# Performance work log

Hardware: AMD Instinct MI355X
Metric: run time of the kernel (lower is better)

The kernel has to match this reference:

```python
import jax, jax.numpy as jnp
import numpy as np

N_HEADS = 16
HEAD_SIZE = 128


def setup_inputs() -> dict:
    key = jax.random.key(0)
    k1, k2, k3 = jax.random.split(key, 3)
    B, S, D = 2, 2048, N_HEADS * HEAD_SIZE
    return {
        "query": jax.random.normal(k1, (B, S, D), dtype=jnp.float32),
        "key": jax.random.normal(k2, (B, S, D), dtype=jnp.float32),
        "value": jax.random.normal(k3, (B, S, D), dtype=jnp.float32),
        "dropout_p": 0,
    }


def reference(query, key, value, dropout_p):
    B, S, D = query.shape
    H, Dh = N_HEADS, HEAD_SIZE
    scale = Dh ** (-0.5)
    q = query.reshape(B, S, H, Dh)
    k = key.reshape(B, S, H, Dh)
    v = value.reshape(B, S, H, Dh)
    # [B, H, Sq, Sk] attention scores
    scores = jnp.einsum("bqhd,bkhd->bhqk", q, k) * scale
    attn = jax.nn.softmax(scores, axis=-1)
    # dropout (deterministic baseline: p == 0 -> identity; inverted dropout otherwise)
    if dropout_p > 0:
        keep = 1.0 - dropout_p
        mask = jax.random.bernoulli(jax.random.key(42), keep, attn.shape)
        attn = jnp.where(mask, attn / keep, 0.0)
    out = jnp.einsum("bhqk,bkhd->bqhd", attn, v)
    return out.reshape(B, S, D)
```

## Files before the change

### kernel.cpp

```cpp
#include <hip/hip_runtime.h>
#include <hip/hip_bf16.h>

#define SEQ   2048
#define DD    2048
#define DH    128
#define NH    16
#define QBLK  128
#define KVBLK 64
#define NT    (SEQ / KVBLK)
#define NWAVE 8
#define BLK   (NWAVE * 64)

#define KSTR  136
#define VSTR  68
#define PSTR  72

typedef __attribute__((ext_vector_type(8))) short bf16x8;
typedef __attribute__((ext_vector_type(4))) short bf16x4;
typedef __attribute__((ext_vector_type(4))) float f32x4;
typedef __attribute__((ext_vector_type(4))) unsigned int u32x4;

__device__ __forceinline__ unsigned int cvt2(float lo, float hi) {
    __hip_bfloat162 h = __float22bfloat162_rn(make_float2(lo, hi));
    unsigned int u;
    __builtin_memcpy(&u, &h, 4);
    return u;
}

__device__ __forceinline__ u32x4 pack8(const float4 a, const float4 b) {
    u32x4 v;
    v[0] = cvt2(a.x, a.y);
    v[1] = cvt2(a.z, a.w);
    v[2] = cvt2(b.x, b.y);
    v[3] = cvt2(b.z, b.w);
    return v;
}

__device__ __forceinline__ unsigned short f2bf1(float f) {
    __hip_bfloat16 h = __float2bfloat16(f);
    unsigned short u;
    __builtin_memcpy(&u, &h, 2);
    return u;
}

__global__ __launch_bounds__(BLK, 4)
void fa_fwd(const float* __restrict__ qg, const float* __restrict__ kg,
            const float* __restrict__ vg, float* __restrict__ og) {
    __shared__ __align__(16) unsigned short Klds[KVBLK * KSTR];
    __shared__ __align__(16) unsigned short Vt[DH * VSTR];
    __shared__ __align__(16) unsigned short Plds[NWAVE * 16 * PSTR];

    const int tid  = threadIdx.x;
    const int w    = tid >> 6;
    const int lane = tid & 63;
    const int lo   = lane & 15;
    const int hi   = lane >> 4;

    const int bid = blockIdx.x;
    const int qt  = bid & 15;
    const int bh  = bid >> 4;
    const int b   = bh >> 4;
    const int h   = bh & 15;
    const int q0  = qt * QBLK;

    const size_t base = (size_t)b * SEQ * DD + (size_t)h * DH;

    bf16x8 qf[4];
    {
        const float* qp = qg + base + (size_t)(q0 + w * 16 + lo) * DD + hi * 8;
        #pragma unroll
        for (int kc = 0; kc < 4; ++kc) {
            float4 a = *(const float4*)(qp + kc * 32);
            float4 c = *(const float4*)(qp + kc * 32 + 4);
            qf[kc] = __builtin_bit_cast(bf16x8, pack8(a, c));
        }
    }

    f32x4 acco[8];
    const f32x4 zf = {0.f, 0.f, 0.f, 0.f};
    #pragma unroll
    for (int i = 0; i < 8; ++i) acco[i] = zf;
    float mrun[4] = {-1e30f, -1e30f, -1e30f, -1e30f};
    float lrun[4] = {0.f, 0.f, 0.f, 0.f};

    const float SCL = 0.08838834764831843f * 1.4426950408889634f;

    unsigned short* pw = Plds + w * 16 * PSTR;

    float4 kra[2], krc[2], vra[2], vrb[2];

    #define LOADT(T)                                                            \
        {                                                                       \
            const int k0_ = (T) * KVBLK;                                        \
            _Pragma("unroll")                                                   \
            for (int i = 0; i < 2; ++i) {                                       \
                int s = tid + i * BLK;                                          \
                const float* p = kg + base + (size_t)(k0_ + (s >> 4)) * DD + (s & 15) * 8; \
                kra[i] = *(const float4*)p;                                     \
                krc[i] = *(const float4*)(p + 4);                               \
                const float* pv = vg + base + (size_t)(k0_ + (s >> 5) * 2) * DD + (s & 31) * 4; \
                vra[i] = *(const float4*)pv;                                    \
                vrb[i] = *(const float4*)(pv + DD);                             \
            }                                                                   \
        }

    LOADT(0);

    for (int t = 0; t < NT; ++t) {
        __syncthreads();

        #pragma unroll
        for (int i = 0; i < 2; ++i) {
            int s = tid + i * BLK;
            *(u32x4*)&Klds[(s >> 4) * KSTR + (s & 15) * 8] = pack8(kra[i], krc[i]);
        }
        #pragma unroll
        for (int i = 0; i < 2; ++i) {
            int s  = tid + i * BLK;
            int kp = s >> 5;
            int c4 = s & 31;
            unsigned int w0 = cvt2(vra[i].x, vrb[i].x);
            unsigned int w1 = cvt2(vra[i].y, vrb[i].y);
            unsigned int w2 = cvt2(vra[i].z, vrb[i].z);
            unsigned int w3 = cvt2(vra[i].w, vrb[i].w);
            unsigned short* vt0 = &Vt[(c4 * 4) * VSTR + kp * 2];
            *(unsigned int*)(vt0)            = w0;
            *(unsigned int*)(vt0 + VSTR)     = w1;
            *(unsigned int*)(vt0 + 2 * VSTR) = w2;
            *(unsigned int*)(vt0 + 3 * VSTR) = w3;
        }

        if (t + 1 < NT) LOADT(t + 1);

        __syncthreads();

        f32x4 accs[4];
        #pragma unroll
        for (int nt = 0; nt < 4; ++nt) accs[nt] = zf;
        #pragma unroll
        for (int nt = 0; nt < 4; ++nt) {
            #pragma unroll
            for (int kk = 0; kk < 4; ++kk) {
                bf16x8 kb = *(const bf16x8*)&Klds[(nt * 16 + lo) * KSTR + kk * 32 + hi * 8];
                accs[nt] = __builtin_amdgcn_mfma_f32_16x16x32_bf16(qf[kk], kb, accs[nt], 0, 0, 0);
            }
        }

        float ps[4][4];
        float corr[4];
        #pragma unroll
        for (int r = 0; r < 4; ++r) {
            float s0 = accs[0][r] * SCL, s1 = accs[1][r] * SCL;
            float s2 = accs[2][r] * SCL, s3 = accs[3][r] * SCL;
            float tm = fmaxf(fmaxf(s0, s1), fmaxf(s2, s3));
            tm = fmaxf(tm, __shfl_xor(tm, 1));
            tm = fmaxf(tm, __shfl_xor(tm, 2));
            tm = fmaxf(tm, __shfl_xor(tm, 4));
            tm = fmaxf(tm, __shfl_xor(tm, 8));
            float mn = fmaxf(mrun[r], tm);
            float c  = exp2f(mrun[r] - mn);
            float p0 = exp2f(s0 - mn), p1 = exp2f(s1 - mn);
            float p2 = exp2f(s2 - mn), p3 = exp2f(s3 - mn);
            float ls = p0 + p1 + p2 + p3;
            ls += __shfl_xor(ls, 1);
            ls += __shfl_xor(ls, 2);
            ls += __shfl_xor(ls, 4);
            ls += __shfl_xor(ls, 8);
            lrun[r] = lrun[r] * c + ls;
            mrun[r] = mn;
            corr[r] = c;
            ps[0][r] = p0; ps[1][r] = p1; ps[2][r] = p2; ps[3][r] = p3;
        }
        #pragma unroll
        for (int d0 = 0; d0 < 8; ++d0) {
            acco[d0][0] *= corr[0]; acco[d0][1] *= corr[1];
            acco[d0][2] *= corr[2]; acco[d0][3] *= corr[3];
        }

        #pragma unroll
        for (int nt = 0; nt < 4; ++nt)
            #pragma unroll
            for (int r = 0; r < 4; ++r)
                pw[(hi * 4 + r) * PSTR + nt * 16 + lo] = f2bf1(ps[nt][r]);

        #pragma unroll
        for (int kc = 0; kc < 2; ++kc) {
            bf16x8 pa = *(const bf16x8*)&pw[lo * PSTR + kc * 32 + hi * 8];
            #pragma unroll
            for (int d0 = 0; d0 < 8; ++d0) {
                const unsigned short* vp = &Vt[(d0 * 16 + lo) * VSTR + kc * 32 + hi * 8];
                bf16x4 v0 = *(const bf16x4*)vp;
                bf16x4 v1 = *(const bf16x4*)(vp + 4);
                bf16x8 vb = __builtin_shufflevector(v0, v1, 0, 1, 2, 3, 4, 5, 6, 7);
                acco[d0] = __builtin_amdgcn_mfma_f32_16x16x32_bf16(pa, vb, acco[d0], 0, 0, 0);
            }
        }
    }

    float inv[4];
    #pragma unroll
    for (int r = 0; r < 4; ++r) inv[r] = 1.0f / lrun[r];
    float* op = og + base + (size_t)(q0 + w * 16 + hi * 4) * DD + lo;
    #pragma unroll
    for (int d0 = 0; d0 < 8; ++d0)
        #pragma unroll
        for (int r = 0; r < 4; ++r)
            op[(size_t)r * DD + d0 * 16] = acco[d0][r] * inv[r];
}

extern "C" void kernel_launch(void* const* d_in, const int* in_sizes, int n_in,
                              void* d_out, int out_size, void* d_ws, size_t ws_size,
                              hipStream_t stream) {
    const float* q = (const float*)d_in[0];
    const float* k = (const float*)d_in[1];
    const float* v = (const float*)d_in[2];
    float* o = (float*)d_out;
    const int B = in_sizes[0] / (SEQ * DD);
    dim3 grid(B * NH * (SEQ / QBLK));
    fa_fwd<<<grid, dim3(BLK), 0, stream>>>(q, k, v, o);
}
```

Before: 338.7 us.

## Process two 16-row query groups per wave with four waves per block

Each block drops from eight waves to four, and each wave now handles 32 query rows as two 16-row groups. Every K and V fragment read from LDS therefore feeds two MFMAs instead of one, halving LDS read traffic per unit of math. Each thread also stages twice as many K/V elements per tile. The cost is more registers per thread (two output accumulator sets, Q fragments and softmax state), so the launch bound drops to 2 blocks per CU, which may reduce occupancy and latency hiding.

```diff
diff --git a/kernel.cpp b/kernel.cpp
--- a/kernel.cpp
+++ b/kernel.cpp
@@ -8,7 +8,7 @@
 #define QBLK  128
 #define KVBLK 64
 #define NT    (SEQ / KVBLK)
-#define NWAVE 8
+#define NWAVE 4
 #define BLK   (NWAVE * 64)
 
 #define KSTR  136
@@ -43,12 +43,12 @@
     return u;
 }
 
-__global__ __launch_bounds__(BLK, 4)
+__global__ __launch_bounds__(BLK, 2)
 void fa_fwd(const float* __restrict__ qg, const float* __restrict__ kg,
             const float* __restrict__ vg, float* __restrict__ og) {
     __shared__ __align__(16) unsigned short Klds[KVBLK * KSTR];
     __shared__ __align__(16) unsigned short Vt[DH * VSTR];
-    __shared__ __align__(16) unsigned short Plds[NWAVE * 16 * PSTR];
+    __shared__ __align__(16) unsigned short Plds[NWAVE * 32 * PSTR];
 
     const int tid  = threadIdx.x;
     const int w    = tid >> 6;
@@ -65,35 +65,41 @@
 
     const size_t base = (size_t)b * SEQ * DD + (size_t)h * DH;
 
-    bf16x8 qf[4];
-    {
-        const float* qp = qg + base + (size_t)(q0 + w * 16 + lo) * DD + hi * 8;
+    bf16x8 qf[2][4];
+    #pragma unroll
+    for (int g = 0; g < 2; ++g) {
+        const float* qp = qg + base + (size_t)(q0 + w * 32 + g * 16 + lo) * DD + hi * 8;
         #pragma unroll
         for (int kc = 0; kc < 4; ++kc) {
             float4 a = *(const float4*)(qp + kc * 32);
             float4 c = *(const float4*)(qp + kc * 32 + 4);
-            qf[kc] = __builtin_bit_cast(bf16x8, pack8(a, c));
+            qf[g][kc] = __builtin_bit_cast(bf16x8, pack8(a, c));
         }
     }
 
-    f32x4 acco[8];
+    f32x4 acco[2][8];
     const f32x4 zf = {0.f, 0.f, 0.f, 0.f};
     #pragma unroll
-    for (int i = 0; i < 8; ++i) acco[i] = zf;
-    float mrun[4] = {-1e30f, -1e30f, -1e30f, -1e30f};
-    float lrun[4] = {0.f, 0.f, 0.f, 0.f};
+    for (int g = 0; g < 2; ++g)
+        #pragma unroll
+        for (int i = 0; i < 8; ++i) acco[g][i] = zf;
+    float mrun[2][4], lrun[2][4];
+    #pragma unroll
+    for (int g = 0; g < 2; ++g)
+        #pragma unroll
+        for (int r = 0; r < 4; ++r) { mrun[g][r] = -1e30f; lrun[g][r] = 0.f; }
 
     const float SCL = 0.08838834764831843f * 1.4426950408889634f;
 
-    unsigned short* pw = Plds + w * 16 * PSTR;
-
-    float4 kra[2], krc[2], vra[2], vrb[2];
+    unsigned short* pw = Plds + w * 32 * PSTR;
+
+    float4 kra[4], krc[4], vra[4], vrb[4];
 
     #define LOADT(T)                                                            \
         {                                                                       \
             const int k0_ = (T) * KVBLK;                                        \
             _Pragma("unroll")                                                   \
-            for (int i = 0; i < 2; ++i) {                                       \
+            for (int i = 0; i < 4; ++i) {                                       \
                 int s = tid + i * BLK;                                          \
                 const float* p = kg + base + (size_t)(k0_ + (s >> 4)) * DD + (s & 15) * 8; \
                 kra[i] = *(const float4*)p;                                     \
@@ -110,12 +116,12 @@
         __syncthreads();
 
         #pragma unroll
-        for (int i = 0; i < 2; ++i) {
+        for (int i = 0; i < 4; ++i) {
             int s = tid + i * BLK;
             *(u32x4*)&Klds[(s >> 4) * KSTR + (s & 15) * 8] = pack8(kra[i], krc[i]);
         }
         #pragma unroll
-        for (int i = 0; i < 2; ++i) {
+        for (int i = 0; i < 4; ++i) {
             int s  = tid + i * BLK;
             int kp = s >> 5;
             int c4 = s & 31;
@@ -134,78 +140,88 @@
 
         __syncthreads();
 
-        f32x4 accs[4];
-        #pragma unroll
-        for (int nt = 0; nt < 4; ++nt) accs[nt] = zf;
+        f32x4 accs[2][4];
+        #pragma unroll
+        for (int g = 0; g < 2; ++g)
+            #pragma unroll
+            for (int nt = 0; nt < 4; ++nt) accs[g][nt] = zf;
         #pragma unroll
         for (int nt = 0; nt < 4; ++nt) {
             #pragma unroll
             for (int kk = 0; kk < 4; ++kk) {
                 bf16x8 kb = *(const bf16x8*)&Klds[(nt * 16 + lo) * KSTR + kk * 32 + hi * 8];
-                accs[nt] = __builtin_amdgcn_mfma_f32_16x16x32_bf16(qf[kk], kb, accs[nt], 0, 0, 0);
-            }
-        }
-
-        float ps[4][4];
-        float corr[4];
-        #pragma unroll
-        for (int r = 0; r < 4; ++r) {
-            float s0 = accs[0][r] * SCL, s1 = accs[1][r] * SCL;
-            float s2 = accs[2][r] * SCL, s3 = accs[3][r] * SCL;
-            float tm = fmaxf(fmaxf(s0, s1), fmaxf(s2, s3));
-            tm = fmaxf(tm, __shfl_xor(tm, 1));
-            tm = fmaxf(tm, __shfl_xor(tm, 2));
-            tm = fmaxf(tm, __shfl_xor(tm, 4));
-            tm = fmaxf(tm, __shfl_xor(tm, 8));
-            float mn = fmaxf(mrun[r], tm);
-            float c  = exp2f(mrun[r] - mn);
-            float p0 = exp2f(s0 - mn), p1 = exp2f(s1 - mn);
-            float p2 = exp2f(s2 - mn), p3 = exp2f(s3 - mn);
-            float ls = p0 + p1 + p2 + p3;
-            ls += __shfl_xor(ls, 1);
-            ls += __shfl_xor(ls, 2);
-            ls += __shfl_xor(ls, 4);
-            ls += __shfl_xor(ls, 8);
-            lrun[r] = lrun[r] * c + ls;
-            mrun[r] = mn;
-            corr[r] = c;
-            ps[0][r] = p0; ps[1][r] = p1; ps[2][r] = p2; ps[3][r] = p3;
-        }
-        #pragma unroll
-        for (int d0 = 0; d0 < 8; ++d0) {
-            acco[d0][0] *= corr[0]; acco[d0][1] *= corr[1];
-            acco[d0][2] *= corr[2]; acco[d0][3] *= corr[3];
-        }
-
-        #pragma unroll
-        for (int nt = 0; nt < 4; ++nt)
-            #pragma unroll
-            for (int r = 0; r < 4; ++r)
-                pw[(hi * 4 + r) * PSTR + nt * 16 + lo] = f2bf1(ps[nt][r]);
+                accs[0][nt] = __builtin_amdgcn_mfma_f32_16x16x32_bf16(qf[0][kk], kb, accs[0][nt], 0, 0, 0);
+                accs[1][nt] = __builtin_amdgcn_mfma_f32_16x16x32_bf16(qf[1][kk], kb, accs[1][nt], 0, 0, 0);
+            }
+        }
+
+        #pragma unroll
+        for (int g = 0; g < 2; ++g) {
+            float ps[4][4];
+            float corr[4];
+            #pragma unroll
+            for (int r = 0; r < 4; ++r) {
+                float s0 = accs[g][0][r] * SCL, s1 = accs[g][1][r] * SCL;
+                float s2 = accs[g][2][r] * SCL, s3 = accs[g][3][r] * SCL;
+                float tm = fmaxf(fmaxf(s0, s1), fmaxf(s2, s3));
+                tm = fmaxf(tm, __shfl_xor(tm, 1));
+                tm = fmaxf(tm, __shfl_xor(tm, 2));
+                tm = fmaxf(tm, __shfl_xor(tm, 4));
+                tm = fmaxf(tm, __shfl_xor(tm, 8));
+                float mn = fmaxf(mrun[g][r], tm);
+                float c  = exp2f(mrun[g][r] - mn);
+                float p0 = exp2f(s0 - mn), p1 = exp2f(s1 - mn);
+                float p2 = exp2f(s2 - mn), p3 = exp2f(s3 - mn);
+                float ls = p0 + p1 + p2 + p3;
+                ls += __shfl_xor(ls, 1);
+                ls += __shfl_xor(ls, 2);
+                ls += __shfl_xor(ls, 4);
+                ls += __shfl_xor(ls, 8);
+                lrun[g][r] = lrun[g][r] * c + ls;
+                mrun[g][r] = mn;
+                corr[r] = c;
+                ps[0][r] = p0; ps[1][r] = p1; ps[2][r] = p2; ps[3][r] = p3;
+            }
+            #pragma unroll
+            for (int d0 = 0; d0 < 8; ++d0) {
+                acco[g][d0][0] *= corr[0]; acco[g][d0][1] *= corr[1];
+                acco[g][d0][2] *= corr[2]; acco[g][d0][3] *= corr[3];
+            }
+            #pragma unroll
+            for (int nt = 0; nt < 4; ++nt)
+                #pragma unroll
+                for (int r = 0; r < 4; ++r)
+                    pw[(g * 16 + hi * 4 + r) * PSTR + nt * 16 + lo] = f2bf1(ps[nt][r]);
+        }
 
         #pragma unroll
         for (int kc = 0; kc < 2; ++kc) {
-            bf16x8 pa = *(const bf16x8*)&pw[lo * PSTR + kc * 32 + hi * 8];
+            bf16x8 pa0 = *(const bf16x8*)&pw[(lo) * PSTR + kc * 32 + hi * 8];
+            bf16x8 pa1 = *(const bf16x8*)&pw[(16 + lo) * PSTR + kc * 32 + hi * 8];
             #pragma unroll
             for (int d0 = 0; d0 < 8; ++d0) {
                 const unsigned short* vp = &Vt[(d0 * 16 + lo) * VSTR + kc * 32 + hi * 8];
                 bf16x4 v0 = *(const bf16x4*)vp;
                 bf16x4 v1 = *(const bf16x4*)(vp + 4);
                 bf16x8 vb = __builtin_shufflevector(v0, v1, 0, 1, 2, 3, 4, 5, 6, 7);
-                acco[d0] = __builtin_amdgcn_mfma_f32_16x16x32_bf16(pa, vb, acco[d0], 0, 0, 0);
+                acco[0][d0] = __builtin_amdgcn_mfma_f32_16x16x32_bf16(pa0, vb, acco[0][d0], 0, 0, 0);
+                acco[1][d0] = __builtin_amdgcn_mfma_f32_16x16x32_bf16(pa1, vb, acco[1][d0], 0, 0, 0);
             }
         }
     }
 
-    float inv[4];
-    #pragma unroll
-    for (int r = 0; r < 4; ++r) inv[r] = 1.0f / lrun[r];
-    float* op = og + base + (size_t)(q0 + w * 16 + hi * 4) * DD + lo;
-    #pragma unroll
-    for (int d0 = 0; d0 < 8; ++d0)
-        #pragma unroll
-        for (int r = 0; r < 4; ++r)
-            op[(size_t)r * DD + d0 * 16] = acco[d0][r] * inv[r];
+    #pragma unroll
+    for (int g = 0; g < 2; ++g) {
+        float inv[4];
+        #pragma unroll
+        for (int r = 0; r < 4; ++r) inv[r] = 1.0f / lrun[g][r];
+        float* op = og + base + (size_t)(q0 + w * 32 + g * 16 + hi * 4) * DD + lo;
+        #pragma unroll
+        for (int d0 = 0; d0 < 8; ++d0)
+            #pragma unroll
+            for (int r = 0; r < 4; ++r)
+                op[(size_t)r * DD + d0 * 16] = acco[g][d0][r] * inv[r];
+    }
 }
 
 extern "C" void kernel_launch(void* const* d_in, const int* in_sizes, int n_in,
```

New measurement: 385.2 us. 13.7% more time.
